# Performance work log

Measured on AMD Instinct MI355X. Metric: run time of the kernel, lower is better.

The kernel has to match this reference:

```python
import jax, jax.numpy as jnp
from jax import lax
import numpy as np

WS = 8      # window_size
SS = 4      # shift_size
NH = 8      # num_heads
DIM = 192
HID = int(DIM * 2.66)  # 510


def _rel_pos_index(ws):
    coords = np.stack(np.meshgrid(np.arange(ws), np.arange(ws), indexing='ij'))
    flat = coords.reshape(2, -1)
    rel = (flat[:, :, None] - flat[:, None, :]).transpose(1, 2, 0)
    rel[..., 0] += ws - 1
    rel[..., 1] += ws - 1
    rel[..., 0] *= 2 * ws - 1
    return rel.sum(-1)  # (ws*ws, ws*ws) int


def _attn_mask(Hp, Wp, ws, ss):
    img = np.zeros((Hp, Wp), dtype=np.float32)
    slices = (slice(0, -ws), slice(-ws, -ss), slice(-ss, None))
    cnt = 0
    for h in slices:
        for w in slices:
            img[h, w] = cnt
            cnt += 1
    mw = img.reshape(Hp // ws, ws, Wp // ws, ws).transpose(0, 2, 1, 3).reshape(-1, ws * ws)
    am = mw[:, None, :] - mw[:, :, None]
    return np.where(am != 0, -100.0, 0.0).astype(np.float32)  # (nW, N, N)


def _ln(t, w, b):
    mu = t.mean(-1, keepdims=True)
    var = t.var(-1, keepdims=True)
    return (t - mu) / jnp.sqrt(var + 1e-5) * w + b


def setup_inputs() -> dict:
    key = jax.random.key(0)
    ks = jax.random.split(key, 12)
    s = 0.05
    return {
        'x': jax.random.normal(ks[0], (2, DIM, 256, 256), jnp.float32),
        'norm1_w': jnp.ones((DIM,), jnp.float32),
        'norm1_b': jnp.zeros((DIM,), jnp.float32),
        'qkv_w': jax.random.normal(ks[1], (3 * DIM, DIM), jnp.float32) * s,
        'rpb_table': jax.random.normal(ks[2], ((2 * WS - 1) * (2 * WS - 1), NH), jnp.float32) * 0.02,
        'proj_w': jax.random.normal(ks[3], (DIM, DIM), jnp.float32) * s,
        'proj_b': jnp.zeros((DIM,), jnp.float32),
        'norm2_w': jnp.ones((DIM,), jnp.float32),
        'norm2_b': jnp.zeros((DIM,), jnp.float32),
        'pin_w': jax.random.normal(ks[4], (2 * HID, DIM), jnp.float32) * s,
        'dw_w': jax.random.normal(ks[5], (2 * HID, 1, 3, 3), jnp.float32) * s,
        'pout_w': jax.random.normal(ks[6], (DIM, HID), jnp.float32) * s,
    }


def reference(x, norm1_w, norm1_b, qkv_w, rpb_table, proj_w, proj_b,
              norm2_w, norm2_b, pin_w, dw_w, pout_w):
    B, C, H, W = x.shape
    hd = C // NH
    scale = hd ** -0.5

    # ---- norm1 (channel-last layernorm) ----
    xc = jnp.transpose(x, (0, 2, 3, 1))  # BHWC
    xn = _ln(xc, norm1_w, norm1_b)

    # ---- pad to window multiple ----
    pad_b = (WS - H % WS) % WS
    pad_r = (WS - W % WS) % WS
    xn = jnp.pad(xn, ((0, 0), (0, pad_b), (0, pad_r), (0, 0)))
    Hp, Wp = H + pad_b, W + pad_r

    # ---- cyclic shift ----
    sx = jnp.roll(xn, (-SS, -SS), axis=(1, 2))

    # ---- window partition ----
    nH, nW = Hp // WS, Wp // WS
    N = WS * WS
    xw = sx.reshape(B, nH, WS, nW, WS, C).transpose(0, 1, 3, 2, 4, 5)
    xw = xw.reshape(B * nH * nW, N, C)

    # ---- window attention ----
    qkv = (xw @ qkv_w.T).reshape(-1, N, 3, NH, hd).transpose(2, 0, 3, 1, 4)
    q, k, v = qkv[0] * scale, qkv[1], qkv[2]  # (B_, NH, N, hd)
    attn = jnp.einsum('bhnd,bhmd->bhnm', q, k)

    idx = _rel_pos_index(WS)
    bias = rpb_table[idx.reshape(-1)].reshape(N, N, NH).transpose(2, 0, 1)
    attn = attn + bias[None]

    mask = jnp.asarray(_attn_mask(Hp, Wp, WS, SS))  # (nWtot, N, N)
    nWtot = nH * nW
    attn = attn.reshape(B, nWtot, NH, N, N) + mask[None, :, None]
    attn = jax.nn.softmax(attn.reshape(-1, NH, N, N), axis=-1)

    out = jnp.einsum('bhnm,bhmd->bhnd', attn, v)
    out = out.transpose(0, 2, 1, 3).reshape(-1, N, C)
    out = out @ proj_w.T + proj_b

    # ---- window reverse + unshift + crop ----
    out = out.reshape(B, nH, nW, WS, WS, C).transpose(0, 1, 3, 2, 4, 5)
    out = out.reshape(B, Hp, Wp, C)
    out = jnp.roll(out, (SS, SS), axis=(1, 2))[:, :H, :W]
    x = x + jnp.transpose(out, (0, 3, 1, 2))

    # ---- FFN: 1x1 in -> depthwise 3x3 -> gated gelu -> 1x1 out ----
    y = _ln(jnp.transpose(x, (0, 2, 3, 1)), norm2_w, norm2_b)
    y = jnp.transpose(y, (0, 3, 1, 2))
    y = jnp.einsum('bchw,oc->bohw', y, pin_w)
    y = lax.conv_general_dilated(y, dw_w, (1, 1), 'SAME',
                                 feature_group_count=dw_w.shape[0],
                                 dimension_numbers=('NCHW', 'OIHW', 'NCHW'))
    h = dw_w.shape[0] // 2
    y = jax.nn.gelu(y[:, :h], approximate=False) * y[:, h:]
    y = jnp.einsum('bchw,oc->bohw', y, pout_w)
    return x + y
```

## Files before the change

kernel.cpp:

```cpp
#include <hip/hip_runtime.h>
#include <hip/hip_bf16.h>
#include <math.h>

#define CDIM 192
#define NTOK 131072
#define HD 24
#define NHEADS 8
#define NTC 65536

typedef __attribute__((ext_vector_type(4))) float floatx4;
typedef __attribute__((ext_vector_type(8))) short bf16x8;
typedef __attribute__((ext_vector_type(4))) unsigned int uintx4;

static __device__ __forceinline__ float bf2f(__hip_bfloat16 h) { return __bfloat162float(h); }
static __device__ __forceinline__ __hip_bfloat16 f2bf(float f) { return __float2bfloat16(f); }
static __device__ __forceinline__ float s2f(short s) {
  union { unsigned u; float f; } c; c.u = ((unsigned)(unsigned short)s) << 16; return c.f;
}
static __device__ __forceinline__ short f2s(float f) {
  __hip_bfloat16 h = __float2bfloat16(f);
  union { __hip_bfloat16 h; short s; } c; c.h = h; return c.s;
}
static __device__ __forceinline__ void load_lds16(const void* g, void* l) {
  __builtin_amdgcn_global_load_lds(
      (const __attribute__((address_space(1))) void*)g,
      (__attribute__((address_space(3))) void*)l, 16, 0, 0);
}

__global__ __launch_bounds__(256) void kcvt(
    const float* __restrict__ in, __hip_bfloat16* __restrict__ out, int n) {
  int i = blockIdx.x * 256 + threadIdx.x;
  if (i < n) out[i] = f2bf(in[i]);
}

__global__ __launch_bounds__(256) void k0_padpout(
    const float* __restrict__ w, __hip_bfloat16* __restrict__ o) {
  int idx = blockIdx.x * 256 + threadIdx.x;
  int n = idx >> 9, k = idx & 511;
  o[idx] = (k < 510) ? f2bf(w[n * 510 + k]) : f2bf(0.f);
}

__global__ __launch_bounds__(256) void k0_padpin(
    const float* __restrict__ w, const float* __restrict__ nw,
    __hip_bfloat16* __restrict__ o) {
  int idx = blockIdx.x * 256 + threadIdx.x;
  int n = idx / 192, k = idx % 192;
  int src = (n < 510) ? n : ((n >= 512 && n < 1022) ? n - 2 : -1);
  o[idx] = (src >= 0) ? f2bf(w[src * 192 + k] * nw[k]) : f2bf(0.f);
}

__global__ __launch_bounds__(256) void k0_st(
    const float* __restrict__ w, const float* __restrict__ nw,
    const float* __restrict__ nb, float* __restrict__ S, float* __restrict__ T) {
  int n = blockIdx.x * 256 + threadIdx.x;
  int src = (n < 510) ? n : ((n >= 512 && n < 1022) ? n - 2 : -1);
  float s = 0.f, t = 0.f;
  if (src >= 0)
    for (int c = 0; c < 192; ++c) {
      float v = w[src * 192 + c];
      s += v * nw[c]; t += v * nb[c];
    }
  S[n] = s; T[n] = t;
}

__global__ __launch_bounds__(256) void k0_wtap(
    const float* __restrict__ wdw, __hip_bfloat16* __restrict__ wa,
    __hip_bfloat16* __restrict__ wg) {
  int idx = blockIdx.x * 256 + threadIdx.x;
  if (idx >= 9 * 512) return;
  int tap = idx >> 9, c = idx & 511;
  wa[idx] = (c < 510) ? f2bf(wdw[c * 9 + tap]) : f2bf(0.f);
  wg[idx] = (c < 510) ? f2bf(wdw[(c + 510) * 9 + tap]) : f2bf(0.f);
}

__global__ __launch_bounds__(256) void k1_ln_raster(
    const float* __restrict__ x,
    const float* __restrict__ w,
    const float* __restrict__ bsh,
    __hip_bfloat16* __restrict__ out) {
  __shared__ float xs[32][193];
  __shared__ float wls[192], bls[192];
  int bid = blockIdx.x;
  int b = bid >> 11, si = (bid >> 3) & 255, sj0 = (bid & 7) << 5;
  int i = (si + 4) & 255;
  int tid = threadIdx.x;
  int lane = tid & 63, wv = tid >> 6;
  if (tid < 192) { wls[tid] = w[tid]; bls[tid] = bsh[tid]; }
  int p0 = (lane & 7) << 2;
  int cb = wv * 8 + (lane >> 3);
  int j4 = (sj0 + p0 + 4) & 255;
  long pbase = ((long)(b * CDIM + cb) << 16) + (i << 8) + j4;
  #pragma unroll
  for (int co = 0; co < 6; ++co) {
    floatx4 v = *(const floatx4*)(x + pbase + ((long)co << 21));
    int c = co * 32 + cb;
    xs[p0 + 0][c] = v[0];
    xs[p0 + 1][c] = v[1];
    xs[p0 + 2][c] = v[2];
    xs[p0 + 3][c] = v[3];
  }
  __syncthreads();
  int p = tid >> 3, q = tid & 7, c0 = q * 24;
  float v[24], s = 0.f, sq = 0.f;
  #pragma unroll
  for (int e = 0; e < 24; ++e) {
    float t = xs[p][c0 + e]; v[e] = t; s += t; sq += t * t;
  }
  #pragma unroll
  for (int off = 1; off < 8; off <<= 1) { s += __shfl_xor(s, off); sq += __shfl_xor(sq, off); }
  float mean = s * (1.0f / 192.0f);
  float var  = sq * (1.0f / 192.0f) - mean * mean;
  float rstd = rsqrtf(var + 1e-5f);
  unsigned pk[12];
  #pragma unroll
  for (int e = 0; e < 12; ++e) {
    unsigned lo = (unsigned short)f2s((v[2*e  ] - mean) * rstd * wls[c0 + 2*e  ] + bls[c0 + 2*e  ]);
    unsigned hi = (unsigned short)f2s((v[2*e+1] - mean) * rstd * wls[c0 + 2*e+1] + bls[c0 + 2*e+1]);
    pk[e] = lo | (hi << 16);
  }
  long tok0 = ((long)b << 16) + (si << 8) + sj0;
  char* gout = (char*)out + (tok0 + p) * 384 + q * 48;
  *(uintx4*)(gout     ) = (uintx4){pk[0], pk[1], pk[2], pk[3]};
  *(uintx4*)(gout + 16) = (uintx4){pk[4], pk[5], pk[6], pk[7]};
  *(uintx4*)(gout + 32) = (uintx4){pk[8], pk[9], pk[10], pk[11]};
}

template <int WM, int WN, int EPI>
__global__ __launch_bounds__(256) void gemm_lds(
    const __hip_bfloat16* __restrict__ A,
    const __hip_bfloat16* __restrict__ B,
    const float* __restrict__ bias,
    __hip_bfloat16* __restrict__ C,
    int K, int lda, int ldb, int ldc) {
  constexpr int BM = 32 * WM, BN = 32 * WN;
  __shared__ __hip_bfloat16 As[BM * 32];
  __shared__ __hip_bfloat16 Bs[BN * 32];
  int t = threadIdx.x;
  int wave = t >> 6, lane = t & 63;
  int wm = wave >> 1, wn = wave & 1;
  int r16 = lane & 15, quad = lane >> 4;
  long m0 = (long)blockIdx.y * BM;
  long n0 = (long)blockIdx.x * BN;
  int srow = t >> 2, scol = (t & 3) << 3;
  floatx4 acc[WM][WN];
  for (int i = 0; i < WM; ++i)
    for (int j = 0; j < WN; ++j)
      acc[i][j] = (floatx4){0.f, 0.f, 0.f, 0.f};
  for (int k0 = 0; k0 < K; k0 += 32) {
    __syncthreads();
    for (int p = 0; p < WM / 2; ++p)
      load_lds16(A + (m0 + srow + p * 64) * lda + k0 + scol,
                 (char*)As + t * 16 + p * 4096);
    for (int p = 0; p < WN / 2; ++p)
      load_lds16(B + (n0 + srow + p * 64) * ldb + k0 + scol,
                 (char*)Bs + t * 16 + p * 4096);
    __syncthreads();
    bf16x8 af[WM], bf[WN];
    for (int i = 0; i < WM; ++i)
      af[i] = *(const bf16x8*)&As[(wm * 16 * WM + i * 16 + r16) * 32 + quad * 8];
    for (int j = 0; j < WN; ++j)
      bf[j] = *(const bf16x8*)&Bs[(wn * 16 * WN + j * 16 + r16) * 32 + quad * 8];
    for (int i = 0; i < WM; ++i)
      for (int j = 0; j < WN; ++j)
        acc[i][j] = __builtin_amdgcn_mfma_f32_16x16x32_bf16(af[i], bf[j], acc[i][j], 0, 0, 0);
  }
  for (int i = 0; i < WM; ++i)
    for (int j = 0; j < WN; ++j) {
      int col = n0 + wn * 16 * WN + j * 16 + r16;
      float badd = (EPI == 1) ? bias[col] : 0.f;
      for (int r = 0; r < 4; ++r) {
        long row = m0 + wm * 16 * WM + i * 16 + quad * 4 + r;
        C[row * ldc + col] = f2bf(acc[i][j][r] + badd);
      }
    }
}

__global__ __launch_bounds__(256) void gemm_pin(
    const __hip_bfloat16* __restrict__ x2,
    const __hip_bfloat16* __restrict__ B,
    const float* __restrict__ stats,
    const float* __restrict__ Sv,
    const float* __restrict__ Tv,
    __hip_bfloat16* __restrict__ C,
    int bb, int r0) {
  constexpr int WM = 4, WN = 4, BM = 128, BN = 128;
  __shared__ __hip_bfloat16 As[BM * 32];
  __shared__ __hip_bfloat16 Bs[BN * 32];
  int t = threadIdx.x;
  int wave = t >> 6, lane = t & 63;
  int wm = wave >> 1, wn = wave & 1;
  int r16 = lane & 15, quad = lane >> 4;
  int m0 = blockIdx.y * BM;
  int n0 = blockIdx.x * BN;
  int srow = t >> 2, scol = (t & 3) << 3;
  floatx4 acc[WM][WN];
  for (int i = 0; i < WM; ++i)
    for (int j = 0; j < WN; ++j)
      acc[i][j] = (floatx4){0.f, 0.f, 0.f, 0.f};
  for (int k0 = 0; k0 < 192; k0 += 32) {
    __syncthreads();
    for (int p = 0; p < 2; ++p) {
      int rr = m0 + srow + p * 64;
      int il = rr >> 8, jj = rr & 255;
      int gi = r0 - 1 + il; gi = gi < 0 ? 0 : (gi > 255 ? 255 : gi);
      long tok = ((long)bb << 16) + (gi << 8) + jj;
      load_lds16(x2 + tok * 192 + k0 + scol, (char*)As + t * 16 + p * 4096);
    }
    for (int p = 0; p < 2; ++p)
      load_lds16(B + (n0 + srow + p * 64) * 192 + k0 + scol,
                 (char*)Bs + t * 16 + p * 4096);
    __syncthreads();
    bf16x8 af[WM], bf[WN];
    for (int i = 0; i < WM; ++i)
      af[i] = *(const bf16x8*)&As[(wm * 64 + i * 16 + r16) * 32 + quad * 8];
    for (int j = 0; j < WN; ++j)
      bf[j] = *(const bf16x8*)&Bs[(wn * 64 + j * 16 + r16) * 32 + quad * 8];
    for (int i = 0; i < WM; ++i)
      for (int j = 0; j < WN; ++j)
        acc[i][j] = __builtin_amdgcn_mfma_f32_16x16x32_bf16(af[i], bf[j], acc[i][j], 0, 0, 0);
  }
  for (int i = 0; i < WM; ++i) {
    float mr[4], rsd[4];
    #pragma unroll
    for (int r = 0; r < 4; ++r) {
      int row = m0 + wm * 64 + i * 16 + quad * 4 + r;
      int il = row >> 8, jj = row & 255;
      int gi = r0 - 1 + il; gi = gi < 0 ? 0 : (gi > 255 ? 255 : gi);
      long tok = ((long)bb << 16) + (gi << 8) + jj;
      mr[r] = stats[2 * tok]; rsd[r] = stats[2 * tok + 1];
    }
    for (int j = 0; j < WN; ++j) {
      int col = n0 + wn * 64 + j * 16 + r16;
      float sv = Sv[col], tv = Tv[col];
      for (int r = 0; r < 4; ++r) {
        int row = m0 + wm * 64 + i * 16 + quad * 4 + r;
        C[(long)row * 1024 + col] = f2bf(acc[i][j][r] * rsd[r] - mr[r] * rsd[r] * sv + tv);
      }
    }
  }
}

__global__ __launch_bounds__(256) void gemm_pout(
    const __hip_bfloat16* __restrict__ A,
    const __hip_bfloat16* __restrict__ B,
    const __hip_bfloat16* __restrict__ x2,
    float* __restrict__ out,
    int b, int r0) {
  constexpr int WM = 2, WN = 4, BM = 64, BN = 128;
  __shared__ __hip_bfloat16 As[BM * 32];
  __shared__ __hip_bfloat16 Bs[BN * 32];
  int t = threadIdx.x;
  int wave = t >> 6, lane = t & 63;
  int wm = wave >> 1, wn = wave & 1;
  int r16 = lane & 15, quad = lane >> 4;
  long m0 = (long)blockIdx.y * BM;
  long n0 = (long)blockIdx.x * BN;
  int srow = t >> 2, scol = (t & 3) << 3;
  floatx4 acc[WM][WN];
  for (int i = 0; i < WM; ++i)
    for (int j = 0; j < WN; ++j)
      acc[i][j] = (floatx4){0.f, 0.f, 0.f, 0.f};
  for (int k0 = 0; k0 < 512; k0 += 32) {
    __syncthreads();
    load_lds16(A + (m0 + srow) * 512 + k0 + scol, (char*)As + t * 16);
    for (int p = 0; p < WN / 2; ++p)
      load_lds16(B + (n0 + srow + p * 64) * 512 + k0 + scol,
                 (char*)Bs + t * 16 + p * 4096);
    __syncthreads();
    bf16x8 af[WM], bf[WN];
    for (int i = 0; i < WM; ++i)
      af[i] = *(const bf16x8*)&As[(wm * 16 * WM + i * 16 + r16) * 32 + quad * 8];
    for (int j = 0; j < WN; ++j)
      bf[j] = *(const bf16x8*)&Bs[(wn * 16 * WN + j * 16 + r16) * 32 + quad * 8];
    for (int i = 0; i < WM; ++i)
      for (int j = 0; j < WN; ++j)
        acc[i][j] = __builtin_amdgcn_mfma_f32_16x16x32_bf16(af[i], bf[j], acc[i][j], 0, 0, 0);
  }
  for (int i = 0; i < WM; ++i)
    for (int j = 0; j < WN; ++j) {
      int p_ = n0 + wn * 16 * WN + j * 16 + r16;
      int il = p_ >> 8, jj = p_ & 255;
      long pix = ((long)(r0 + il) << 8) + jj;
      for (int r = 0; r < 4; ++r) {
        int c_ = m0 + wm * 16 * WM + i * 16 + quad * 4 + r;
        long tok = ((long)b << 16) + pix;
        float v = acc[i][j][r] + bf2f(x2[tok * CDIM + c_]);
        out[((long)(b * CDIM + c_) << 16) + pix] = v;
      }
    }
}

__global__ __launch_bounds__(256) void k3_attn(
    const __hip_bfloat16* __restrict__ qkv,
    const float* __restrict__ rpb,
    __hip_bfloat16* __restrict__ out,
    int wid0) {
  __shared__ alignas(16) short Kp[64 * 32];
  __shared__ alignas(16) short Vt[32 * 64];
  __shared__ alignas(16) short Ps[4][16 * 64];
  __shared__ float rpbs[225];
  int bidx = blockIdx.x;
  int h = (bidx >> 3) & 7;
  int widl = ((bidx >> 6) << 3) | (bidx & 7);
  int wid = wid0 + widl;
  int t = threadIdx.x;
  int wv = t >> 6, lane = t & 63, quad = lane >> 4, r16 = lane & 15;
  int wi_l = widl >> 5, wjl = widl & 31;
  const short* qk = (const short*)qkv;

  if (t < 225) rpbs[t] = rpb[t * NHEADS + h];

  {
    int kr = t >> 2, kq = t & 3;
    bf16x8 kv = {0, 0, 0, 0, 0, 0, 0, 0};
    if (kq < 3) {
      long ltok = (long)((((wi_l << 3) + (kr >> 3)) << 8) + (wjl << 3) + (kr & 7));
      kv = *(const bf16x8*)(qk + ltok * 576 + 192 + h * HD + kq * 8);
    }
    *(bf16x8*)&Kp[kr * 32 + ((kq ^ ((kr >> 1) & 3)) << 3)] = kv;
  }
  {
    int tok = t & 63, q8 = t >> 6;
    if (q8 < 3) {
      long ltok = (long)((((wi_l << 3) + (tok >> 3)) << 8) + (wjl << 3) + (tok & 7));
      bf16x8 vv = *(const bf16x8*)(qk + ltok * 576 + 384 + h * HD + q8 * 8);
      #pragma unroll
      for (int e = 0; e < 8; ++e) {
        int d = q8 * 8 + e;
        Vt[d * 64 + (((tok >> 3) ^ (d & 7)) << 3) + (tok & 7)] = vv[e];
      }
    } else {
      int zt = t - 192;
      int d = 24 + (zt >> 3), tokg = zt & 7;
      bf16x8 z = {0, 0, 0, 0, 0, 0, 0, 0};
      *(bf16x8*)&Vt[d * 64 + ((tokg ^ (d & 7)) << 3)] = z;
    }
  }
  bf16x8 qf = {0, 0, 0, 0, 0, 0, 0, 0};
  if (quad < 3) {
    int nn = wv * 16 + r16;
    long ltok = (long)((((wi_l << 3) + (nn >> 3)) << 8) + (wjl << 3) + (nn & 7));
    qf = *(const bf16x8*)(qk + ltok * 576 + h * HD + quad * 8);
  }
  __syncthreads();

  floatx4 sj[4];
  int kswz = (quad ^ ((r16 >> 1) & 3)) << 3;
  #pragma unroll
  for (int j = 0; j < 4; ++j) {
    bf16x8 kf = *(const bf16x8*)&Kp[(j * 16 + r16) * 32 + kswz];
    sj[j] = __builtin_amdgcn_mfma_f32_16x16x32_bf16(
        qf, kf, (floatx4){0.f, 0.f, 0.f, 0.f}, 0, 0, 0);
  }

  int b = wid >> 10, wi = (wid >> 5) & 31, wj = wid & 31;
  int rkj[4];
  #pragma unroll
  for (int j = 0; j < 4; ++j) {
    int m = j * 16 + r16;
    int gsi = wi * 8 + (m >> 3), gsj = wj * 8 + (m & 7);
    rkj[j] = ((gsi < 248) ? 0 : (gsi < 252 ? 1 : 2)) * 3 +
             ((gsj < 248) ? 0 : (gsj < 252 ? 1 : 2));
  }

  float rs[4];
  #pragma unroll
  for (int r = 0; r < 4; ++r) {
    int n = wv * 16 + quad * 4 + r;
    int ti = n >> 3, tj = n & 7;
    int gi = wi * 8 + ti, gj = wj * 8 + tj;
    int rq = ((gi < 248) ? 0 : (gi < 252 ? 1 : 2)) * 3 +
             ((gj < 248) ? 0 : (gj < 252 ? 1 : 2));
    float val[4];
    float mx = -1e30f;
    #pragma unroll
    for (int j = 0; j < 4; ++j) {
      int m = j * 16 + r16;
      int idx = (ti - (m >> 3) + 7) * 15 + (tj - (m & 7) + 7);
      float v = sj[j][r] * 0.20412414523193154f + rpbs[idx];
      if (rkj[j] != rq) v -= 100.0f;
      val[j] = v;
      mx = fmaxf(mx, v);
    }
    #pragma unroll
    for (int off = 1; off < 16; off <<= 1) mx = fmaxf(mx, __shfl_xor(mx, off));
    float sum = 0.f;
    int row = quad * 4 + r;
    #pragma unroll
    for (int j = 0; j < 4; ++j) {
      float p = __expf(val[j] - mx);
      sum += p;
      int col = j * 16 + r16;
      Ps[wv][row * 64 + ((((col >> 3) ^ (row & 7)) << 3)) + (col & 7)] = f2s(p);
    }
    #pragma unroll
    for (int off = 1; off < 16; off <<= 1) sum += __shfl_xor(sum, off);
    rs[r] = 1.0f / sum;
  }
  __syncthreads();

  floatx4 o0 = {0.f, 0.f, 0.f, 0.f}, o1 = {0.f, 0.f, 0.f, 0.f};
  #pragma unroll
  for (int kk = 0; kk < 2; ++kk) {
    int g = (((kk * 4 + quad) ^ (r16 & 7)) << 3);
    bf16x8 pa = *(const bf16x8*)&Ps[wv][r16 * 64 + g];
    bf16x8 b0 = *(const bf16x8*)&Vt[r16 * 64 + g];
    bf16x8 b1 = *(const bf16x8*)&Vt[(16 + r16) * 64 + g];
    o0 = __builtin_amdgcn_mfma_f32_16x16x32_bf16(pa, b0, o0, 0, 0, 0);
    o1 = __builtin_amdgcn_mfma_f32_16x16x32_bf16(pa, b1, o1, 0, 0, 0);
  }
  #pragma unroll
  for (int r = 0; r < 4; ++r) {
    int n = wv * 16 + quad * 4 + r;
    int gi = wi * 8 + (n >> 3), gj = wj * 8 + (n & 7);
    long ob = (((long)b << 16) + (gi << 8) + gj) * CDIM + h * HD;
    out[ob + r16] = f2bf(o0[r] * rs[r]);
    if (r16 < 8) out[ob + 16 + r16] = f2bf(o1[r] * rs[r]);
  }
}

__global__ __launch_bounds__(256) void k4_res_raster(
    const float* __restrict__ x,
    const __hip_bfloat16* __restrict__ tmp,
    __hip_bfloat16* __restrict__ x2,
    float* __restrict__ stats) {
  __shared__ float xs[32][193];
  int bid = blockIdx.x;
  int b = bid >> 11, i = (bid >> 3) & 255, j0 = (bid & 7) << 5;
  int tid = threadIdx.x;
  int lane = tid & 63, wv = tid >> 6;
  int p0 = (lane & 7) << 2;
  int cb = wv * 8 + (lane >> 3);
  long pbase = ((long)(b * CDIM + cb) << 16) + (i << 8) + j0 + p0;
  #pragma unroll
  for (int co = 0; co < 6; ++co) {
    floatx4 v = *(const floatx4*)(x + pbase + ((long)co << 21));
    int c = co * 32 + cb;
    xs[p0 + 0][c] = v[0];
    xs[p0 + 1][c] = v[1];
    xs[p0 + 2][c] = v[2];
    xs[p0 + 3][c] = v[3];
  }
  __syncthreads();
  int p = tid >> 3, q = tid & 7, c0 = q * 24;
  int j = j0 + p;
  int si = (i + 252) & 255, sj = (j + 252) & 255;
  long tsh = ((long)b << 16) + (si << 8) + sj;
  const short* tp = (const short*)tmp + tsh * 192 + c0;
  bf16x8 t0 = *(const bf16x8*)(tp);
  bf16x8 t1 = *(const bf16x8*)(tp + 8);
  bf16x8 t2v = *(const bf16x8*)(tp + 16);
  float v[24], s = 0.f, sq = 0.f;
  #pragma unroll
  for (int e = 0; e < 8; ++e) {
    float a0 = xs[p][c0 + e     ] + s2f(t0[e]);
    float a1 = xs[p][c0 + e + 8 ] + s2f(t1[e]);
    float a2 = xs[p][c0 + e + 16] + s2f(t2v[e]);
    v[e] = a0; v[e + 8] = a1; v[e + 16] = a2;
    s += a0 + a1 + a2;
    sq += a0 * a0 + a1 * a1 + a2 * a2;
  }
  #pragma unroll
  for (int off = 1; off < 8; off <<= 1) { s += __shfl_xor(s, off); sq += __shfl_xor(sq, off); }
  float mean = s * (1.0f / 192.0f);
  float var  = sq * (1.0f / 192.0f) - mean * mean;
  float rstd = rsqrtf(var + 1e-5f);
  long t2g = ((long)b << 16) + (i << 8) + j;
  if (q == 0) { stats[2 * t2g] = mean; stats[2 * t2g + 1] = rstd; }
  unsigned pk[12];
  #pragma unroll
  for (int e = 0; e < 12; ++e) {
    unsigned lo = (unsigned short)f2s(v[2 * e]);
    unsigned hi = (unsigned short)f2s(v[2 * e + 1]);
    pk[e] = lo | (hi << 16);
  }
  char* gout = (char*)x2 + t2g * 384 + q * 48;
  *(uintx4*)(gout     ) = (uintx4){pk[0], pk[1], pk[2], pk[3]};
  *(uintx4*)(gout + 16) = (uintx4){pk[4], pk[5], pk[6], pk[7]};
  *(uintx4*)(gout + 32) = (uintx4){pk[8], pk[9], pk[10], pk[11]};
}

__global__ __launch_bounds__(256) void k7_dwgate(
    const __hip_bfloat16* __restrict__ pin,
    const __hip_bfloat16* __restrict__ wa,
    const __hip_bfloat16* __restrict__ wg,
    __hip_bfloat16* __restrict__ out,
    int r0) {
  int t = threadIdx.x;
  int oct = t & 63, pl = t >> 6;
  int p = blockIdx.x * 4 + pl;
  int il = p >> 8, j = p & 255;
  int gi = r0 + il;
  int c0 = oct << 3;
  float a[8], g[8];
  for (int e = 0; e < 8; ++e) { a[e] = 0.f; g[e] = 0.f; }
  for (int di = -1; di <= 1; ++di) {
    int ii = gi + di; if (ii < 0 || ii > 255) continue;
    int br = il + di + 1;
    for (int dj = -1; dj <= 1; ++dj) {
      int jj = j + dj; if (jj < 0 || jj > 255) continue;
      long nbase = ((long)((br << 8) + jj)) << 10;
      int tap = (di + 1) * 3 + (dj + 1);
      bf16x8 va  = *(const bf16x8*)((const short*)pin + nbase + c0);
      bf16x8 vg  = *(const bf16x8*)((const short*)pin + nbase + 512 + c0);
      bf16x8 wa8 = *(const bf16x8*)((const short*)wa + tap * 512 + c0);
      bf16x8 wg8 = *(const bf16x8*)((const short*)wg + tap * 512 + c0);
      for (int e = 0; e < 8; ++e) {
        a[e] += s2f(wa8[e]) * s2f(va[e]);
        g[e] += s2f(wg8[e]) * s2f(vg[e]);
      }
    }
  }
  bf16x8 r;
  for (int e = 0; e < 8; ++e) {
    float ge = 0.5f * a[e] * (1.0f + erff(a[e] * 0.70710678118654752f));
    r[e] = f2s(ge * g[e]);
  }
  *(bf16x8*)((short*)out + (long)p * 512 + c0) = r;
}

extern "C" void kernel_launch(void* const* d_in, const int* in_sizes, int n_in,
                              void* d_out, int out_size, void* d_ws, size_t ws_size,
                              hipStream_t stream) {
  const float* x       = (const float*)d_in[0];
  const float* norm1_w = (const float*)d_in[1];
  const float* norm1_b = (const float*)d_in[2];
  const float* qkv_w   = (const float*)d_in[3];
  const float* rpb     = (const float*)d_in[4];
  const float* proj_w  = (const float*)d_in[5];
  const float* proj_b  = (const float*)d_in[6];
  const float* norm2_w = (const float*)d_in[7];
  const float* norm2_b = (const float*)d_in[8];
  const float* pin_w   = (const float*)d_in[9];
  const float* dw_w    = (const float*)d_in[10];
  const float* pout_w  = (const float*)d_in[11];

  char* ws = (char*)d_ws;
  __hip_bfloat16* wsLN1 = (__hip_bfloat16*)(ws);
  __hip_bfloat16* wsPRJ = (__hip_bfloat16*)(ws);
  __hip_bfloat16* wsPINC= (__hip_bfloat16*)(ws);
  __hip_bfloat16* wsATT = (__hip_bfloat16*)(ws + 50331648UL);
  __hip_bfloat16* wsX2  = (__hip_bfloat16*)(ws + 50331648UL);
  float*          wsST  = (float*)         (ws + 100663296UL);
  __hip_bfloat16* wsGT  = (__hip_bfloat16*)(ws + 101711872UL);
  __hip_bfloat16* wsWA  = (__hip_bfloat16*)(ws + 118489088UL);
  __hip_bfloat16* wsWG  = (__hip_bfloat16*)(ws + 118507520UL);
  float*          wsS   = (float*)         (ws + 118517760UL);
  float*          wsT   = (float*)         (ws + 118525952UL);
  __hip_bfloat16* wsPW  = (__hip_bfloat16*)(ws + 120586240UL);
  __hip_bfloat16* wsQW  = (__hip_bfloat16*)(ws + 120782848UL);
  __hip_bfloat16* wsPJW = (__hip_bfloat16*)(ws + 121004032UL);
  __hip_bfloat16* wsPIW = (__hip_bfloat16*)(ws + 121077760UL);
  float* out = (float*)d_out;
  __hip_bfloat16* qkvbuf = (__hip_bfloat16*)d_out;

  kcvt<<<(110592 + 255) / 256, 256, 0, stream>>>(qkv_w, wsQW, 110592);
  kcvt<<<(36864 + 255) / 256, 256, 0, stream>>>(proj_w, wsPJW, 36864);
  k0_padpout<<<384, 256, 0, stream>>>(pout_w, wsPW);
  k0_padpin<<<768, 256, 0, stream>>>(pin_w, norm2_w, wsPIW);
  k0_st<<<4, 256, 0, stream>>>(pin_w, norm2_w, norm2_b, wsS, wsT);
  k0_wtap<<<18, 256, 0, stream>>>(dw_w, wsWA, wsWG);
  k1_ln_raster<<<4096, 256, 0, stream>>>(x, norm1_w, norm1_b, wsLN1);
  for (int b = 0; b < 2; ++b) {
    gemm_lds<4, 2, 0><<<dim3(9, 512), 256, 0, stream>>>(
        wsLN1 + (long)b * 65536 * CDIM, wsQW, nullptr, qkvbuf, 192, 192, 192, 576);
    k3_attn<<<8192, 256, 0, stream>>>(qkvbuf, rpb, wsATT, b * 1024);
  }
  gemm_lds<4, 2, 1><<<dim3(3, 1024), 256, 0, stream>>>(
      wsATT, wsPJW, proj_b, wsPRJ, 192, 192, 192, 192);
  k4_res_raster<<<4096, 256, 0, stream>>>(x, wsPRJ, wsX2, wsST);
  for (int cc = 0; cc < 8; ++cc) {
    int b = cc >> 2, r0 = (cc & 3) * 64;
    gemm_pin<<<dim3(8, 132), 256, 0, stream>>>(
        wsX2, wsPIW, wsST, wsS, wsT, wsPINC, b, r0);
    k7_dwgate<<<4096, 256, 0, stream>>>(wsPINC, wsWA, wsWG, wsGT, r0);
    gemm_pout<<<dim3(128, 3), 256, 0, stream>>>(wsPW, wsGT, wsX2, out, b, r0);
  }
}
```

Baseline: 890.0 us.

## Compute two pixels per thread in dwgate and enlarge GEMM M-tiles

```diff
diff --git a/kernel.cpp b/kernel.cpp
--- a/kernel.cpp
+++ b/kernel.cpp
@@ -487,36 +487,62 @@
     __hip_bfloat16* __restrict__ out,
     int r0) {
   int t = threadIdx.x;
-  int oct = t & 63, pl = t >> 6;
-  int p = blockIdx.x * 4 + pl;
-  int il = p >> 8, j = p & 255;
+  int oct = t & 63, s = t >> 6;
+  int p0 = blockIdx.x * 8 + s * 2;
+  int il = p0 >> 8, j0 = p0 & 255;
   int gi = r0 + il;
   int c0 = oct << 3;
-  float a[8], g[8];
-  for (int e = 0; e < 8; ++e) { a[e] = 0.f; g[e] = 0.f; }
-  for (int di = -1; di <= 1; ++di) {
-    int ii = gi + di; if (ii < 0 || ii > 255) continue;
-    int br = il + di + 1;
-    for (int dj = -1; dj <= 1; ++dj) {
-      int jj = j + dj; if (jj < 0 || jj > 255) continue;
-      long nbase = ((long)((br << 8) + jj)) << 10;
-      int tap = (di + 1) * 3 + (dj + 1);
-      bf16x8 va  = *(const bf16x8*)((const short*)pin + nbase + c0);
-      bf16x8 vg  = *(const bf16x8*)((const short*)pin + nbase + 512 + c0);
-      bf16x8 wa8 = *(const bf16x8*)((const short*)wa + tap * 512 + c0);
-      bf16x8 wg8 = *(const bf16x8*)((const short*)wg + tap * 512 + c0);
-      for (int e = 0; e < 8; ++e) {
-        a[e] += s2f(wa8[e]) * s2f(va[e]);
-        g[e] += s2f(wg8[e]) * s2f(vg[e]);
+  bf16x8 Wa[9], Wg[9];
+  #pragma unroll
+  for (int tap = 0; tap < 9; ++tap) {
+    Wa[tap] = *(const bf16x8*)((const short*)wa + tap * 512 + c0);
+    Wg[tap] = *(const bf16x8*)((const short*)wg + tap * 512 + c0);
+  }
+  bool rv0 = (gi - 1) >= 0, rv2 = (gi + 1) <= 255;
+  float a0[8], g0[8], a1[8], g1[8];
+  #pragma unroll
+  for (int e = 0; e < 8; ++e) { a0[e] = 0.f; g0[e] = 0.f; a1[e] = 0.f; g1[e] = 0.f; }
+  #pragma unroll
+  for (int k = 0; k < 4; ++k) {
+    int c = j0 - 1 + k;
+    bool cv = (c >= 0) && (c <= 255);
+    #pragma unroll
+    for (int di = 0; di < 3; ++di) {
+      bool valid = cv && (di == 0 ? rv0 : (di == 2 ? rv2 : true));
+      bf16x8 va = {0, 0, 0, 0, 0, 0, 0, 0}, vg = {0, 0, 0, 0, 0, 0, 0, 0};
+      if (valid) {
+        long nbase = ((long)(((il + di) << 8) + c)) << 10;
+        va = *(const bf16x8*)((const short*)pin + nbase + c0);
+        vg = *(const bf16x8*)((const short*)pin + nbase + 512 + c0);
       }
-    }
-  }
-  bf16x8 r;
+      if (k <= 2) {
+        int tap = di * 3 + k;
+        #pragma unroll
+        for (int e = 0; e < 8; ++e) {
+          a0[e] += s2f(Wa[tap][e]) * s2f(va[e]);
+          g0[e] += s2f(Wg[tap][e]) * s2f(vg[e]);
+        }
+      }
+      if (k >= 1) {
+        int tap = di * 3 + k - 1;
+        #pragma unroll
+        for (int e = 0; e < 8; ++e) {
+          a1[e] += s2f(Wa[tap][e]) * s2f(va[e]);
+          g1[e] += s2f(Wg[tap][e]) * s2f(vg[e]);
+        }
+      }
+    }
+  }
+  bf16x8 r0v, r1v;
+  #pragma unroll
   for (int e = 0; e < 8; ++e) {
-    float ge = 0.5f * a[e] * (1.0f + erff(a[e] * 0.70710678118654752f));
-    r[e] = f2s(ge * g[e]);
-  }
-  *(bf16x8*)((short*)out + (long)p * 512 + c0) = r;
+    float ge0 = 0.5f * a0[e] * (1.0f + erff(a0[e] * 0.70710678118654752f));
+    float ge1 = 0.5f * a1[e] * (1.0f + erff(a1[e] * 0.70710678118654752f));
+    r0v[e] = f2s(ge0 * g0[e]);
+    r1v[e] = f2s(ge1 * g1[e]);
+  }
+  *(bf16x8*)((short*)out + (long)p0 * 512 + c0) = r0v;
+  *(bf16x8*)((short*)out + (long)(p0 + 1) * 512 + c0) = r1v;
 }
 
 extern "C" void kernel_launch(void* const* d_in, const int* in_sizes, int n_in,
@@ -562,18 +588,18 @@
   k0_wtap<<<18, 256, 0, stream>>>(dw_w, wsWA, wsWG);
   k1_ln_raster<<<4096, 256, 0, stream>>>(x, norm1_w, norm1_b, wsLN1);
   for (int b = 0; b < 2; ++b) {
-    gemm_lds<4, 2, 0><<<dim3(9, 512), 256, 0, stream>>>(
+    gemm_lds<8, 2, 0><<<dim3(9, 256), 256, 0, stream>>>(
         wsLN1 + (long)b * 65536 * CDIM, wsQW, nullptr, qkvbuf, 192, 192, 192, 576);
     k3_attn<<<8192, 256, 0, stream>>>(qkvbuf, rpb, wsATT, b * 1024);
   }
-  gemm_lds<4, 2, 1><<<dim3(3, 1024), 256, 0, stream>>>(
+  gemm_lds<8, 2, 1><<<dim3(3, 512), 256, 0, stream>>>(
       wsATT, wsPJW, proj_b, wsPRJ, 192, 192, 192, 192);
   k4_res_raster<<<4096, 256, 0, stream>>>(x, wsPRJ, wsX2, wsST);
   for (int cc = 0; cc < 8; ++cc) {
     int b = cc >> 2, r0 = (cc & 3) * 64;
     gemm_pin<<<dim3(8, 132), 256, 0, stream>>>(
         wsX2, wsPIW, wsST, wsS, wsT, wsPINC, b, r0);
-    k7_dwgate<<<4096, 256, 0, stream>>>(wsPINC, wsWA, wsWG, wsGT, r0);
+    k7_dwgate<<<2048, 256, 0, stream>>>(wsPINC, wsWA, wsWG, wsGT, r0);
     gemm_pout<<<dim3(128, 3), 256, 0, stream>>>(wsPW, wsGT, wsX2, out, b, r0);
   }
 }
```

New measurement: 890.1 us. About the same (+0.0%).
